# Performance work log

Measured on AMD Instinct MI355X. Metric: run time of the kernel, lower is better.

## Reference

```python
import jax, jax.numpy as jnp
import numpy as np

W_CHAMFER = 1.0
W_SMOOTH = 0.5
K_NEIGHBORS = 8


def _pairwise_sqdist(a, b):
    # a: [B,N,3], b: [B,M,3] -> [B,N,M] squared euclidean distances
    a2 = jnp.sum(a * a, axis=-1)  # [B,N]
    b2 = jnp.sum(b * b, axis=-1)  # [B,M]
    ab = jnp.einsum('bnd,bmd->bnm', a, b)  # [B,N,M]
    d2 = a2[:, :, None] + b2[:, None, :] - 2.0 * ab
    return jnp.maximum(d2, 0.0)


def _chamfer(pc1, pc2):
    d = jnp.sqrt(_pairwise_sqdist(pc1, pc2))  # [B,N,M] euclidean (matches torch.norm)
    d1 = jnp.min(d, axis=2)  # [B,N]
    d2 = jnp.min(d, axis=1)  # [B,M]
    return jnp.mean(d1) + jnp.mean(d2)


def _smoothness(pc, flow, k=K_NEIGHBORS):
    d2 = _pairwise_sqdist(pc, pc)  # [B,N,N]
    # k+1 nearest (squared dist preserves ordering); drop self (index 0)
    _, idx = jax.lax.top_k(-d2, k + 1)  # [B,N,k+1]
    idx = idx[:, :, 1:]  # [B,N,k]
    neighbor_flow = jax.vmap(lambda f, i: f[i])(flow, idx)  # [B,N,k,3]
    diff = flow[:, :, None, :] - neighbor_flow
    return jnp.mean(jnp.linalg.norm(diff, axis=-1))


def setup_inputs() -> dict:
    key = jax.random.key(0)
    k1, k2, k3 = jax.random.split(key, 3)
    B, N, M = 2, 8192, 8192
    pc1 = jax.random.normal(k1, (B, N, 3), dtype=jnp.float32)
    pc2 = jax.random.normal(k2, (B, M, 3), dtype=jnp.float32)
    pred_flow = jax.random.normal(k3, (B, N, 3), dtype=jnp.float32) * 0.1
    return {"pc1": pc1, "pc2": pc2, "pred_flow": pred_flow}


def reference(pc1, pc2, pred_flow):
    pc1_warped = pc1 + pred_flow
    l_chamfer = _chamfer(pc1_warped, pc2)
    l_smooth = _smoothness(pc1, pred_flow)
    return W_CHAMFER * l_chamfer + W_SMOOTH * l_smooth
```

## Files before the change

kernel.cpp:

```cpp
#include <hip/hip_runtime.h>

#define N_PTS 8192
#define BATCH 2
#define KNN 8
#define NBLK_C 1024
#define NBLK_S 1024

#define ARR_PC2  0
#define ARR_WARP 2
#define ARR_PC1  4

__device__ __forceinline__ void ce(unsigned &x, unsigned &y) {
    unsigned lo = min(x, y), hi = max(x, y); x = lo; y = hi;
}

__device__ __forceinline__ void insert4(unsigned o[4], unsigned key) {
    unsigned n0 = min(o[0], key);
    unsigned n1 = max(o[0], min(o[1], key));
    unsigned n2 = max(o[1], min(o[2], key));
    unsigned n3 = max(o[2], min(o[3], key));
    o[0]=n0; o[1]=n1; o[2]=n2; o[3]=n3;
}

__device__ __forceinline__ void merge_stage8(unsigned m[8], int d) {
    unsigned p[8], c[8];
    #pragma unroll
    for (int k = 0; k < 8; ++k) p[k] = (unsigned)__shfl_xor((int)m[k], d, 64);
    #pragma unroll
    for (int k = 0; k < 8; ++k) c[k] = min(m[k], p[7-k]);
    ce(c[0],c[4]); ce(c[1],c[5]); ce(c[2],c[6]); ce(c[3],c[7]);
    ce(c[0],c[2]); ce(c[1],c[3]); ce(c[4],c[6]); ce(c[5],c[7]);
    ce(c[0],c[1]); ce(c[2],c[3]); ce(c[4],c[5]); ce(c[6],c[7]);
    #pragma unroll
    for (int k = 0; k < 8; ++k) m[k] = c[k];
}

__device__ __forceinline__ void merge64(unsigned m[8]) {
    merge_stage8(m, 1); merge_stage8(m, 2); merge_stage8(m, 4);
    merge_stage8(m, 8); merge_stage8(m, 16); merge_stage8(m, 32);
}

__global__ __launch_bounds__(256) void pack_kernel(
        const float* __restrict__ pc1, const float* __restrict__ pc2,
        const float* __restrict__ flow, float4* __restrict__ ws) {
    const int t = blockIdx.x * 256 + threadIdx.x;
    const int arr = t >> 13, i = t & (N_PTS - 1);
    const int bb = arr & 1;
    const size_t base = (size_t)bb * N_PTS * 3 + (size_t)i * 3;
    float x, y, z;
    if (arr < 2)      { x = pc2[base+0];              y = pc2[base+1];              z = pc2[base+2]; }
    else if (arr < 4) { x = pc1[base+0] + flow[base+0];
                        y = pc1[base+1] + flow[base+1];
                        z = pc1[base+2] + flow[base+2]; }
    else              { x = pc1[base+0];              y = pc1[base+1];              z = pc1[base+2]; }
    ws[t] = make_float4(x, y, z, fmaf(x, x, fmaf(y, y, z * z)));
}

__global__ __launch_bounds__(256, 4) void chamfer_kernel(
        const float4* __restrict__ ws, float* __restrict__ out) {
    __shared__ float psum[4];
    const int tid = threadIdx.x, bx = blockIdx.x;
    const int lane = tid & 63, wv = tid >> 6;
    const int z = bx >> 8, bb = z & 1, dir = z >> 1;
    const int cb = bx & 255;
    const float4* rows = ws + (size_t)((dir == 0 ? ARR_WARP : ARR_PC2) + bb) * N_PTS;
    const float4* cand = ws + (size_t)((dir == 0 ? ARR_PC2 : ARR_WARP) + bb) * N_PTS;
    const int rbase = cb * 32 + wv * 8;

    float mx[8], my[8], mz[8], bmin[8];
    #pragma unroll
    for (int k = 0; k < 8; ++k) {
        float4 q = rows[rbase + k];
        mx[k] = -2.0f * q.x; my[k] = -2.0f * q.y; mz[k] = -2.0f * q.z;
        bmin[k] = __builtin_inff();
    }

    #pragma unroll 2
    for (int j = 0; j < N_PTS; j += 128) {
        float4 qa = cand[j + lane];
        float4 qb = cand[j + 64 + lane];
        #pragma unroll
        for (int k = 0; k < 8; ++k) {
            float sa = fmaf(mx[k], qa.x, fmaf(my[k], qa.y, fmaf(mz[k], qa.z, qa.w)));
            float sb = fmaf(mx[k], qb.x, fmaf(my[k], qb.y, fmaf(mz[k], qb.z, qb.w)));
            bmin[k] = fminf(fminf(bmin[k], sa), sb);
        }
    }

    #pragma unroll
    for (int k = 0; k < 8; ++k) {
        #pragma unroll
        for (int d = 1; d < 64; d <<= 1)
            bmin[k] = fminf(bmin[k], __shfl_xor(bmin[k], d, 64));
    }
    if (lane == 0) {
        float val = 0.0f;
        #pragma unroll
        for (int k = 0; k < 8; ++k) {
            float p2k = 0.25f * fmaf(mx[k], mx[k], fmaf(my[k], my[k], mz[k] * mz[k]));
            val += sqrtf(fmaxf(bmin[k] + p2k, 0.0f));
        }
        psum[wv] = val;
    }
    __syncthreads();
    if (tid == 0) {
        float ch = psum[0] + psum[1] + psum[2] + psum[3];
        atomicAdd(out, ch * (1.0f / (float)(BATCH * N_PTS)));
    }
}

__global__ __launch_bounds__(256, 4) void smooth_kernel(
        const float4* __restrict__ ws, const float* __restrict__ flow,
        float* __restrict__ out) {
    __shared__ float psum[4];
    const int tid = threadIdx.x, bx = blockIdx.x;
    const int lane = tid & 63, wv = tid >> 6;
    const int b  = bx >> 9;
    const int sx = bx & 511;
    const int i0w = sx * 16 + wv * 4;
    const float4* cand = ws + (size_t)(ARR_PC1 + b) * N_PTS;
    const float* F = flow + (size_t)b * N_PTS * 3;

    float mx[4], my[4], mz[4], p2[4], gr[4];
    unsigned thr[4], o[4][4];
    #pragma unroll
    for (int r = 0; r < 4; ++r) {
        float4 q = cand[i0w + r];
        mx[r] = -2.0f * q.x; my[r] = -2.0f * q.y; mz[r] = -2.0f * q.z;
        p2[r] = q.w;
        gr[r] = __builtin_inff();
        thr[r] = 0xFFFFFFFFu;
        #pragma unroll
        for (int k = 0; k < 4; ++k) o[r][k] = 0xFFFFFFFFu;
    }

    auto update_thr = [&]() {
        #pragma unroll
        for (int r = 0; r < 4; ++r) {
            unsigned m0 = o[r][0], m1 = o[r][1], m2 = o[r][2], m3 = o[r][3];
            #pragma unroll
            for (int d = 1; d <= 16; d <<= 1) {
                unsigned q0 = (unsigned)__shfl_xor((int)m0, d, 64);
                unsigned q1 = (unsigned)__shfl_xor((int)m1, d, 64);
                unsigned q2 = (unsigned)__shfl_xor((int)m2, d, 64);
                unsigned q3 = (unsigned)__shfl_xor((int)m3, d, 64);
                unsigned c0 = min(m0, q3), c1 = min(m1, q2);
                unsigned c2 = min(m2, q1), c3 = min(m3, q0);
                ce(c0, c2); ce(c1, c3); ce(c0, c1); ce(c2, c3);
                m0 = c0; m1 = c1; m2 = c2; m3 = c3;
            }
            unsigned bound = max(m3, (unsigned)__shfl_xor((int)m3, 32, 64));
            thr[r] = min(thr[r], bound);
            float thr_up = __uint_as_float((thr[r] & 0xFFFFE000u) + 0x4000u);
            gr[r] = thr_up - p2[r];
        }
    };

    auto gated_span = [&](int j0, int j1) {
        #pragma unroll 2
        for (int j = j0; j < j1; j += 64) {
            float4 qa = cand[j + lane];
            int jj = j + lane;
            float sc[4];
            #pragma unroll
            for (int r = 0; r < 4; ++r)
                sc[r] = fmaf(mx[r], qa.x, fmaf(my[r], qa.y, fmaf(mz[r], qa.z, qa.w)));
            #pragma unroll
            for (int r = 0; r < 4; ++r) {
                if (__any(sc[r] <= gr[r])) {
                    float d2 = fmaxf(sc[r] + p2[r], 0.0f);
                    unsigned key = (__float_as_uint(d2) & 0xFFFFE000u) | (unsigned)jj;
                    key = (jj == i0w + r) ? 0xFFFFFFFFu : key;
                    insert4(o[r], key);
                }
            }
        }
    };

    #pragma unroll 4
    for (int j = 0; j < 1024; j += 64) {
        float4 qa = cand[j + lane];
        int jj = j + lane;
        #pragma unroll
        for (int r = 0; r < 4; ++r) {
            float ss = fmaf(mx[r], qa.x, fmaf(my[r], qa.y, fmaf(mz[r], qa.z, qa.w)));
            float d2 = fmaxf(ss + p2[r], 0.0f);
            unsigned key = (__float_as_uint(d2) & 0xFFFFE000u) | (unsigned)jj;
            key = (jj == i0w + r) ? 0xFFFFFFFFu : key;
            insert4(o[r], key);
        }
    }
    update_thr();
    gated_span(1024, 2048); update_thr();
    gated_span(2048, 4096); update_thr();
    gated_span(4096, N_PTS);

    const int sel = lane & 31;
    const int pr = sel >> 3, kk = sel & 7;
    unsigned mykey = 0xFFFFFFFFu;
    #pragma unroll
    for (int r = 0; r < 4; ++r) {
        unsigned m[8] = {o[r][0], o[r][1], o[r][2], o[r][3],
                         0xFFFFFFFFu, 0xFFFFFFFFu, 0xFFFFFFFFu, 0xFFFFFFFFu};
        merge64(m);
        if (pr == r) {
            unsigned k2 = m[0];
            #pragma unroll
            for (int t = 1; t < 8; ++t) k2 = (kk == t) ? m[t] : k2;
            mykey = k2;
        }
    }
    const int i = i0w + pr;
    const int j = (int)(mykey & (N_PTS - 1));
    float dx = F[i*3+0] - F[j*3+0];
    float dy = F[i*3+1] - F[j*3+1];
    float dz = F[i*3+2] - F[j*3+2];
    float sv = sqrtf(fmaf(dx, dx, fmaf(dy, dy, dz * dz)));
    #pragma unroll
    for (int d = 1; d < 64; d <<= 1) sv += __shfl_xor(sv, d, 64);
    if (lane == 0) psum[wv] = sv;
    __syncthreads();

    if (tid == 0) {
        float sm = psum[0] + psum[1] + psum[2] + psum[3];
        atomicAdd(out, sm * (0.25f / ((float)BATCH * N_PTS * KNN)));
    }
}

extern "C" void kernel_launch(void* const* d_in, const int* in_sizes, int n_in,
                              void* d_out, int out_size, void* d_ws, size_t ws_size,
                              hipStream_t stream) {
    const float* pc1  = (const float*)d_in[0];
    const float* pc2  = (const float*)d_in[1];
    const float* flow = (const float*)d_in[2];
    float* out = (float*)d_out;
    float4* ws4 = (float4*)d_ws;

    pack_kernel<<<dim3(6 * N_PTS / 256), 256, 0, stream>>>(pc1, pc2, flow, ws4);
    chamfer_kernel<<<dim3(NBLK_C), 256, 0, stream>>>(ws4, out);
    smooth_kernel<<<dim3(NBLK_S), 256, 0, stream>>>(ws4, flow, out);
}
```

Measured before the change: 155.9 us.

## Fuse chamfer and smoothness kernels into one interleaved launch, halve rows per smooth wave

```diff
diff --git a/kernel.cpp b/kernel.cpp
--- a/kernel.cpp
+++ b/kernel.cpp
@@ -4,7 +4,8 @@
 #define BATCH 2
 #define KNN 8
 #define NBLK_C 1024
-#define NBLK_S 1024
+#define NBLK_S 2048
+#define NBLOCKS (NBLK_C + NBLK_S)
 
 #define ARR_PC2  0
 #define ARR_WARP 2
@@ -56,174 +57,186 @@
     ws[t] = make_float4(x, y, z, fmaf(x, x, fmaf(y, y, z * z)));
 }
 
-__global__ __launch_bounds__(256, 4) void chamfer_kernel(
-        const float4* __restrict__ ws, float* __restrict__ out) {
-    __shared__ float psum[4];
-    const int tid = threadIdx.x, bx = blockIdx.x;
-    const int lane = tid & 63, wv = tid >> 6;
-    const int z = bx >> 8, bb = z & 1, dir = z >> 1;
-    const int cb = bx & 255;
-    const float4* rows = ws + (size_t)((dir == 0 ? ARR_WARP : ARR_PC2) + bb) * N_PTS;
-    const float4* cand = ws + (size_t)((dir == 0 ? ARR_PC2 : ARR_WARP) + bb) * N_PTS;
-    const int rbase = cb * 32 + wv * 8;
-
-    float mx[8], my[8], mz[8], bmin[8];
-    #pragma unroll
-    for (int k = 0; k < 8; ++k) {
-        float4 q = rows[rbase + k];
-        mx[k] = -2.0f * q.x; my[k] = -2.0f * q.y; mz[k] = -2.0f * q.z;
-        bmin[k] = __builtin_inff();
-    }
-
-    #pragma unroll 2
-    for (int j = 0; j < N_PTS; j += 128) {
-        float4 qa = cand[j + lane];
-        float4 qb = cand[j + 64 + lane];
-        #pragma unroll
-        for (int k = 0; k < 8; ++k) {
-            float sa = fmaf(mx[k], qa.x, fmaf(my[k], qa.y, fmaf(mz[k], qa.z, qa.w)));
-            float sb = fmaf(mx[k], qb.x, fmaf(my[k], qb.y, fmaf(mz[k], qb.z, qb.w)));
-            bmin[k] = fminf(fminf(bmin[k], sa), sb);
-        }
-    }
-
-    #pragma unroll
-    for (int k = 0; k < 8; ++k) {
-        #pragma unroll
-        for (int d = 1; d < 64; d <<= 1)
-            bmin[k] = fminf(bmin[k], __shfl_xor(bmin[k], d, 64));
-    }
-    if (lane == 0) {
-        float val = 0.0f;
-        #pragma unroll
-        for (int k = 0; k < 8; ++k) {
-            float p2k = 0.25f * fmaf(mx[k], mx[k], fmaf(my[k], my[k], mz[k] * mz[k]));
-            val += sqrtf(fmaxf(bmin[k] + p2k, 0.0f));
-        }
-        psum[wv] = val;
-    }
-    __syncthreads();
-    if (tid == 0) {
-        float ch = psum[0] + psum[1] + psum[2] + psum[3];
-        atomicAdd(out, ch * (1.0f / (float)(BATCH * N_PTS)));
-    }
-}
-
-__global__ __launch_bounds__(256, 4) void smooth_kernel(
+__global__ __launch_bounds__(256, 4) void mega_kernel(
         const float4* __restrict__ ws, const float* __restrict__ flow,
         float* __restrict__ out) {
     __shared__ float psum[4];
     const int tid = threadIdx.x, bx = blockIdx.x;
     const int lane = tid & 63, wv = tid >> 6;
-    const int b  = bx >> 9;
-    const int sx = bx & 511;
-    const int i0w = sx * 16 + wv * 4;
-    const float4* cand = ws + (size_t)(ARR_PC1 + b) * N_PTS;
-    const float* F = flow + (size_t)b * N_PTS * 3;
-
-    float mx[4], my[4], mz[4], p2[4], gr[4];
-    unsigned thr[4], o[4][4];
-    #pragma unroll
-    for (int r = 0; r < 4; ++r) {
-        float4 q = cand[i0w + r];
-        mx[r] = -2.0f * q.x; my[r] = -2.0f * q.y; mz[r] = -2.0f * q.z;
-        p2[r] = q.w;
-        gr[r] = __builtin_inff();
-        thr[r] = 0xFFFFFFFFu;
-        #pragma unroll
-        for (int k = 0; k < 4; ++k) o[r][k] = 0xFFFFFFFFu;
-    }
-
-    auto update_thr = [&]() {
-        #pragma unroll
-        for (int r = 0; r < 4; ++r) {
-            unsigned m0 = o[r][0], m1 = o[r][1], m2 = o[r][2], m3 = o[r][3];
-            #pragma unroll
-            for (int d = 1; d <= 16; d <<= 1) {
-                unsigned q0 = (unsigned)__shfl_xor((int)m0, d, 64);
-                unsigned q1 = (unsigned)__shfl_xor((int)m1, d, 64);
-                unsigned q2 = (unsigned)__shfl_xor((int)m2, d, 64);
-                unsigned q3 = (unsigned)__shfl_xor((int)m3, d, 64);
-                unsigned c0 = min(m0, q3), c1 = min(m1, q2);
-                unsigned c2 = min(m2, q1), c3 = min(m3, q0);
-                ce(c0, c2); ce(c1, c3); ce(c0, c1); ce(c2, c3);
-                m0 = c0; m1 = c1; m2 = c2; m3 = c3;
-            }
-            unsigned bound = max(m3, (unsigned)__shfl_xor((int)m3, 32, 64));
-            thr[r] = min(thr[r], bound);
-            float thr_up = __uint_as_float((thr[r] & 0xFFFFE000u) + 0x4000u);
-            gr[r] = thr_up - p2[r];
-        }
-    };
-
-    auto gated_span = [&](int j0, int j1) {
+    const int ri = bx / 3, role = bx % 3;
+
+    if (role == 2) {
+        const int z = ri >> 8, bb = z & 1, dir = z >> 1;
+        const int cb = ri & 255;
+        const float4* rows = ws + (size_t)((dir == 0 ? ARR_WARP : ARR_PC2) + bb) * N_PTS;
+        const float4* cand = ws + (size_t)((dir == 0 ? ARR_PC2 : ARR_WARP) + bb) * N_PTS;
+        const int rbase = cb * 32 + wv * 8;
+
+        float mx[8], my[8], mz[8], bmin[8];
+        #pragma unroll
+        for (int k = 0; k < 8; ++k) {
+            float4 q = rows[rbase + k];
+            mx[k] = -2.0f * q.x; my[k] = -2.0f * q.y; mz[k] = -2.0f * q.z;
+            bmin[k] = __builtin_inff();
+        }
+
         #pragma unroll 2
-        for (int j = j0; j < j1; j += 64) {
+        for (int j = 0; j < N_PTS; j += 128) {
             float4 qa = cand[j + lane];
-            int jj = j + lane;
-            float sc[4];
-            #pragma unroll
-            for (int r = 0; r < 4; ++r)
-                sc[r] = fmaf(mx[r], qa.x, fmaf(my[r], qa.y, fmaf(mz[r], qa.z, qa.w)));
-            #pragma unroll
-            for (int r = 0; r < 4; ++r) {
-                if (__any(sc[r] <= gr[r])) {
-                    float d2 = fmaxf(sc[r] + p2[r], 0.0f);
-                    unsigned key = (__float_as_uint(d2) & 0xFFFFE000u) | (unsigned)jj;
-                    key = (jj == i0w + r) ? 0xFFFFFFFFu : key;
-                    insert4(o[r], key);
+            float4 qb = cand[j + 64 + lane];
+            #pragma unroll
+            for (int k = 0; k < 8; ++k) {
+                float sa = fmaf(mx[k], qa.x, fmaf(my[k], qa.y, fmaf(mz[k], qa.z, qa.w)));
+                float sb = fmaf(mx[k], qb.x, fmaf(my[k], qb.y, fmaf(mz[k], qb.z, qb.w)));
+                bmin[k] = fminf(fminf(bmin[k], sa), sb);
+            }
+        }
+
+        #pragma unroll
+        for (int k = 0; k < 8; ++k) {
+            #pragma unroll
+            for (int d = 1; d < 64; d <<= 1)
+                bmin[k] = fminf(bmin[k], __shfl_xor(bmin[k], d, 64));
+        }
+        if (lane == 0) {
+            float val = 0.0f;
+            #pragma unroll
+            for (int k = 0; k < 8; ++k) {
+                float p2k = 0.25f * fmaf(mx[k], mx[k], fmaf(my[k], my[k], mz[k] * mz[k]));
+                val += sqrtf(fmaxf(bmin[k] + p2k, 0.0f));
+            }
+            psum[wv] = val;
+        }
+        __syncthreads();
+        if (tid == 0) {
+            float ch = psum[0] + psum[1] + psum[2] + psum[3];
+            atomicAdd(out, ch * (1.0f / (float)(BATCH * N_PTS)));
+        }
+    } else {
+        const int sbx = ri * 2 + role;
+        const int b  = sbx >> 10;
+        const int sx = sbx & 1023;
+        const int i0w = sx * 8 + wv * 2;
+        const float4* cand = ws + (size_t)(ARR_PC1 + b) * N_PTS;
+        const float* F = flow + (size_t)b * N_PTS * 3;
+
+        float mx[2], my[2], mz[2], p2[2], gr[2];
+        unsigned thr[2], o[2][4];
+        #pragma unroll
+        for (int r = 0; r < 2; ++r) {
+            float4 q = cand[i0w + r];
+            mx[r] = -2.0f * q.x; my[r] = -2.0f * q.y; mz[r] = -2.0f * q.z;
+            p2[r] = q.w;
+            gr[r] = __builtin_inff();
+            thr[r] = 0xFFFFFFFFu;
+            #pragma unroll
+            for (int k = 0; k < 4; ++k) o[r][k] = 0xFFFFFFFFu;
+        }
+
+        auto update_thr = [&]() {
+            #pragma unroll
+            for (int r = 0; r < 2; ++r) {
+                unsigned m0 = o[r][0], m1 = o[r][1], m2 = o[r][2], m3 = o[r][3];
+                #pragma unroll
+                for (int d = 1; d <= 16; d <<= 1) {
+                    unsigned q0 = (unsigned)__shfl_xor((int)m0, d, 64);
+                    unsigned q1 = (unsigned)__shfl_xor((int)m1, d, 64);
+                    unsigned q2 = (unsigned)__shfl_xor((int)m2, d, 64);
+                    unsigned q3 = (unsigned)__shfl_xor((int)m3, d, 64);
+                    unsigned c0 = min(m0, q3), c1 = min(m1, q2);
+                    unsigned c2 = min(m2, q1), c3 = min(m3, q0);
+                    ce(c0, c2); ce(c1, c3); ce(c0, c1); ce(c2, c3);
+                    m0 = c0; m1 = c1; m2 = c2; m3 = c3;
                 }
-            }
-        }
-    };
-
-    #pragma unroll 4
-    for (int j = 0; j < 1024; j += 64) {
-        float4 qa = cand[j + lane];
-        int jj = j + lane;
-        #pragma unroll
-        for (int r = 0; r < 4; ++r) {
-            float ss = fmaf(mx[r], qa.x, fmaf(my[r], qa.y, fmaf(mz[r], qa.z, qa.w)));
-            float d2 = fmaxf(ss + p2[r], 0.0f);
-            unsigned key = (__float_as_uint(d2) & 0xFFFFE000u) | (unsigned)jj;
-            key = (jj == i0w + r) ? 0xFFFFFFFFu : key;
-            insert4(o[r], key);
-        }
-    }
-    update_thr();
-    gated_span(1024, 2048); update_thr();
-    gated_span(2048, 4096); update_thr();
-    gated_span(4096, N_PTS);
-
-    const int sel = lane & 31;
-    const int pr = sel >> 3, kk = sel & 7;
-    unsigned mykey = 0xFFFFFFFFu;
-    #pragma unroll
-    for (int r = 0; r < 4; ++r) {
-        unsigned m[8] = {o[r][0], o[r][1], o[r][2], o[r][3],
-                         0xFFFFFFFFu, 0xFFFFFFFFu, 0xFFFFFFFFu, 0xFFFFFFFFu};
-        merge64(m);
-        if (pr == r) {
-            unsigned k2 = m[0];
-            #pragma unroll
-            for (int t = 1; t < 8; ++t) k2 = (kk == t) ? m[t] : k2;
-            mykey = k2;
-        }
-    }
-    const int i = i0w + pr;
-    const int j = (int)(mykey & (N_PTS - 1));
-    float dx = F[i*3+0] - F[j*3+0];
-    float dy = F[i*3+1] - F[j*3+1];
-    float dz = F[i*3+2] - F[j*3+2];
-    float sv = sqrtf(fmaf(dx, dx, fmaf(dy, dy, dz * dz)));
-    #pragma unroll
-    for (int d = 1; d < 64; d <<= 1) sv += __shfl_xor(sv, d, 64);
-    if (lane == 0) psum[wv] = sv;
-    __syncthreads();
-
-    if (tid == 0) {
-        float sm = psum[0] + psum[1] + psum[2] + psum[3];
-        atomicAdd(out, sm * (0.25f / ((float)BATCH * N_PTS * KNN)));
+                unsigned bound = max(m3, (unsigned)__shfl_xor((int)m3, 32, 64));
+                thr[r] = min(thr[r], bound);
+                float thr_up = __uint_as_float((thr[r] & 0xFFFFE000u) + 0x4000u);
+                gr[r] = thr_up - p2[r];
+            }
+        };
+
+        auto gated_span = [&](int j0, int j1) {
+            #pragma unroll 2
+            for (int j = j0; j < j1; j += 128) {
+                float4 qa = cand[j + lane];
+                float4 qb = cand[j + 64 + lane];
+                int ja = j + lane, jb = j + 64 + lane;
+                float sa[2], sb[2];
+                #pragma unroll
+                for (int r = 0; r < 2; ++r) {
+                    sa[r] = fmaf(mx[r], qa.x, fmaf(my[r], qa.y, fmaf(mz[r], qa.z, qa.w)));
+                    sb[r] = fmaf(mx[r], qb.x, fmaf(my[r], qb.y, fmaf(mz[r], qb.z, qb.w)));
+                }
+                #pragma unroll
+                for (int r = 0; r < 2; ++r) {
+                    if (__any(fminf(sa[r], sb[r]) <= gr[r])) {
+                        float da = fmaxf(sa[r] + p2[r], 0.0f);
+                        unsigned ka = (__float_as_uint(da) & 0xFFFFE000u) | (unsigned)ja;
+                        ka = (ja == i0w + r) ? 0xFFFFFFFFu : ka;
+                        insert4(o[r], ka);
+                        float db = fmaxf(sb[r] + p2[r], 0.0f);
+                        unsigned kb = (__float_as_uint(db) & 0xFFFFE000u) | (unsigned)jb;
+                        kb = (jb == i0w + r) ? 0xFFFFFFFFu : kb;
+                        insert4(o[r], kb);
+                    }
+                }
+            }
+        };
+
+        #pragma unroll 2
+        for (int j = 0; j < 1024; j += 128) {
+            float4 qa = cand[j + lane];
+            float4 qb = cand[j + 64 + lane];
+            int ja = j + lane, jb = j + 64 + lane;
+            #pragma unroll
+            for (int r = 0; r < 2; ++r) {
+                float sa = fmaf(mx[r], qa.x, fmaf(my[r], qa.y, fmaf(mz[r], qa.z, qa.w)));
+                float da = fmaxf(sa + p2[r], 0.0f);
+                unsigned ka = (__float_as_uint(da) & 0xFFFFE000u) | (unsigned)ja;
+                ka = (ja == i0w + r) ? 0xFFFFFFFFu : ka;
+                insert4(o[r], ka);
+                float sb = fmaf(mx[r], qb.x, fmaf(my[r], qb.y, fmaf(mz[r], qb.z, qb.w)));
+                float db = fmaxf(sb + p2[r], 0.0f);
+                unsigned kb = (__float_as_uint(db) & 0xFFFFE000u) | (unsigned)jb;
+                kb = (jb == i0w + r) ? 0xFFFFFFFFu : kb;
+                insert4(o[r], kb);
+            }
+        }
+        update_thr();
+        gated_span(1024, 2048); update_thr();
+        gated_span(2048, 4096); update_thr();
+        gated_span(4096, N_PTS);
+
+        const int sel = lane & 15;
+        const int pr = sel >> 3, kk = sel & 7;
+        unsigned mykey = 0xFFFFFFFFu;
+        #pragma unroll
+        for (int r = 0; r < 2; ++r) {
+            unsigned m[8] = {o[r][0], o[r][1], o[r][2], o[r][3],
+                             0xFFFFFFFFu, 0xFFFFFFFFu, 0xFFFFFFFFu, 0xFFFFFFFFu};
+            merge64(m);
+            if (pr == r) {
+                unsigned k2 = m[0];
+                #pragma unroll
+                for (int t = 1; t < 8; ++t) k2 = (kk == t) ? m[t] : k2;
+                mykey = k2;
+            }
+        }
+        const int i = i0w + pr;
+        const int j = (int)(mykey & (N_PTS - 1));
+        float dx = F[i*3+0] - F[j*3+0];
+        float dy = F[i*3+1] - F[j*3+1];
+        float dz = F[i*3+2] - F[j*3+2];
+        float sv = sqrtf(fmaf(dx, dx, fmaf(dy, dy, dz * dz)));
+        #pragma unroll
+        for (int d = 1; d < 64; d <<= 1) sv += __shfl_xor(sv, d, 64);
+        if (lane == 0) psum[wv] = sv;
+        __syncthreads();
+
+        if (tid == 0) {
+            float sm = psum[0] + psum[1] + psum[2] + psum[3];
+            atomicAdd(out, sm * (0.125f / ((float)BATCH * N_PTS * KNN)));
+        }
     }
 }
 
@@ -237,6 +250,5 @@
     float4* ws4 = (float4*)d_ws;
 
     pack_kernel<<<dim3(6 * N_PTS / 256), 256, 0, stream>>>(pc1, pc2, flow, ws4);
-    chamfer_kernel<<<dim3(NBLK_C), 256, 0, stream>>>(ws4, out);
-    smooth_kernel<<<dim3(NBLK_S), 256, 0, stream>>>(ws4, flow, out);
-}
+    mega_kernel<<<dim3(NBLOCKS), 256, 0, stream>>>(ws4, flow, out);
+}
```

New measurement: 135.8 us. 1.15x faster.
